# Kernel tuning notes

Hardware: AMD Instinct MI355X
Metric: run time of the kernel (lower is better)

The kernel has to match this reference:

```python
import jax, jax.numpy as jnp
import numpy as np

H, C, L = 2, 32, 25
EPS = 1e-5


def setup_inputs() -> dict:
    key = jax.random.key(0)
    ks = jax.random.split(key, 12)
    N, E = 20000, 100000
    x_input = jax.random.normal(ks[0], (N, 5), jnp.float32)
    # edges with no self loops (module uses add_self_loops=True, which first removes them)
    src = jax.random.randint(ks[1], (L, E), 0, N, dtype=jnp.int32)
    off = jax.random.randint(ks[2], (L, E), 1, N, dtype=jnp.int32)
    dst = (src + off) % N
    edge_indices = jnp.stack([src, dst], axis=1)              # [L, 2, E]
    edge_weights = jax.random.uniform(ks[3], (L, E, 1), jnp.float32)
    g = lambda k, shp, fan: jax.random.normal(k, shp, jnp.float32) / np.float32(np.sqrt(fan))
    return {
        "x_input": x_input,
        "edge_indices": edge_indices,
        "edge_weights": edge_weights,
        "Wl": g(ks[4], (L, 5, H * C), 5),
        "bl": jnp.zeros((L, H * C), jnp.float32),
        "Wr": g(ks[5], (L, 5, H * C), 5),
        "br": jnp.zeros((L, H * C), jnp.float32),
        "We": g(ks[6], (L, 1, H * C), 1),
        "att": g(ks[7], (L, H, C), C),
        "conv_bias": jnp.zeros((L, C), jnp.float32),
        "gamma1": jnp.ones((L, C), jnp.float32),
        "beta1": jnp.zeros((L, C), jnp.float32),
        "W1": g(ks[8], (800, 800), 800),
        "b1": jnp.zeros((800,), jnp.float32),
        "W2": g(ks[9], (800, 5), 800),
        "b2": jnp.zeros((5,), jnp.float32),
    }


def reference(x_input, edge_indices, edge_weights, Wl, bl, Wr, br, We, att,
              conv_bias, gamma1, beta1, W1, b1, W2, b2):
    N = x_input.shape[0]
    loops = jnp.arange(N, dtype=edge_indices.dtype)

    def layer(carry, p):
        ei, ew, wl, bl_, wr, br_, we, a, cb, g_, be_ = p
        src, dst = ei[0], ei[1]
        ones_e = jnp.ones((src.shape[0],), x_input.dtype)
        # add_self_loops with fill_value='mean': loop attr = mean of incoming edge attrs
        cnt = jax.ops.segment_sum(ones_e, dst, num_segments=N)
        loop_attr = jax.ops.segment_sum(ew, dst, num_segments=N) / jnp.maximum(cnt, 1.0)[:, None]
        s2 = jnp.concatenate([src, loops])
        d2 = jnp.concatenate([dst, loops])
        ea = jnp.concatenate([ew, loop_attr], axis=0)          # [E+N, 1]
        xl = (x_input @ wl + bl_).reshape(N, H, C)             # source transform
        xr = (x_input @ wr + br_).reshape(N, H, C)             # target transform
        eh = jax.nn.leaky_relu(xl[s2] + xr[d2] + (ea @ we).reshape(-1, H, C), 0.2)
        alpha = jnp.einsum('ehc,hc->eh', eh, a)                # [E+N, H]
        amax = jax.ops.segment_max(alpha, d2, num_segments=N)
        alpha = jnp.exp(alpha - amax[d2])
        alpha = alpha / jax.ops.segment_sum(alpha, d2, num_segments=N)[d2]
        msg = (xl[s2] * alpha[:, :, None]).reshape(-1, H * C)
        deg = jax.ops.segment_sum(jnp.ones((s2.shape[0],), x_input.dtype), d2, num_segments=N)
        out = (jax.ops.segment_sum(msg, d2, num_segments=N) / deg[:, None]).reshape(N, H, C)
        out = out.mean(axis=1) + cb                            # concat=False -> mean over heads, + bias
        mu = out.mean(axis=0)
        var = out.var(axis=0)                                  # BatchNorm1d, training-mode batch stats
        out = g_ * (out - mu) * jax.lax.rsqrt(var + EPS) + be_
        return carry, jax.nn.leaky_relu(out, 0.01)

    _, hs = jax.lax.scan(layer, None,
                         (edge_indices, edge_weights, Wl, bl, Wr, br, We, att,
                          conv_bias, gamma1, beta1))            # [L, N, C]
    h = jnp.transpose(hs, (1, 0, 2)).reshape(N, L * C)          # cat along feature dim
    h = jax.nn.relu(h @ W1 + b1)
    return h @ W2 + b2
```

## Files before the change

### kernel.cpp

```cpp
#include <hip/hip_runtime.h>
#include <hip/hip_bf16.h>

#define N_NODES 20000
#define N_EDGES 100000
#define N_LAYERS 25
#define NPAD 20096
#define EPS_BN 1e-5f
#define LOG2E 1.44269504088896340736f
#define NL_NN (N_LAYERS * N_NODES)
#define TOTAL_E (N_LAYERS * N_EDGES)
#define SCAN_BLKS ((NL_NN + 1023) / 1024)
#define QUARTER_N 5000
#define CNT_BLKS (N_LAYERS * 4)
#define W1T_END (CNT_BLKS + 700)
#define XPAD_END (W1T_END + 157)
#define HPAD_BLKS 75
#define PREP_BLKS (XPAD_END + HPAD_BLKS)
#define EDGE_BLKS ((TOTAL_E + 1023) / 1024)
#define FILL_BLKS (EDGE_BLKS + SCAN_BLKS)
#define NGRP 14
#define ATTN_BLKS (NL_NN / 4)
#define ATTN_PER_XCD (ATTN_BLKS / 8)

typedef short short8 __attribute__((ext_vector_type(8)));
typedef short short4v __attribute__((ext_vector_type(4)));
typedef float floatx4 __attribute__((ext_vector_type(4)));
typedef float float8v __attribute__((ext_vector_type(8)));
typedef int int8v __attribute__((ext_vector_type(8)));
typedef int int2v __attribute__((ext_vector_type(2)));

template <int PAT>
__device__ __forceinline__ float swz(float v) {
  return __int_as_float(__builtin_amdgcn_ds_swizzle(__float_as_int(v), PAT));
}

template <int CTRL>
__device__ __forceinline__ float dpp_add(float v) {
  int r = __builtin_amdgcn_update_dpp(0, __float_as_int(v), CTRL, 0xF, 0xF, true);
  return v + __int_as_float(r);
}

__device__ __forceinline__ float ldbf(const unsigned short* __restrict__ p, int idx) {
  return __uint_as_float((unsigned)p[idx] << 16);
}

__device__ __forceinline__ unsigned short bfbits(float v) {
  return __builtin_bit_cast(unsigned short, (__hip_bfloat16)v);
}

__device__ __forceinline__ void gl_lds16(const short* g, short* l) {
  __builtin_amdgcn_global_load_lds(
      (const __attribute__((address_space(1))) void*)g,
      (__attribute__((address_space(3))) void*)l, 16, 0, 0);
}

__device__ __forceinline__ int8v sload8(const void* p) {
  int8v r;
  asm volatile(
      "s_load_dwordx8 %0, %1, 0x0\n\t"
      "s_waitcnt lgkmcnt(0)"
      : "=s"(r)
      : "s"(p));
  return r;
}

__device__ __forceinline__ void sload2(const void* p, int& a, int& b) {
  int2v r;
  asm volatile(
      "s_load_dwordx2 %0, %1, 0x0\n\t"
      "s_waitcnt lgkmcnt(0)"
      : "=s"(r)
      : "s"(p));
  a = r[0];
  b = r[1];
}

__device__ __forceinline__ void sload_chunk(const void* p, int8v& r0, int8v& r1,
                                            int8v& r2, int8v& r3) {
  asm volatile(
      "s_load_dwordx8 %0, %4, 0x0\n\t"
      "s_load_dwordx8 %1, %4, 0x20\n\t"
      "s_load_dwordx8 %2, %4, 0x40\n\t"
      "s_load_dwordx8 %3, %4, 0x60\n\t"
      "s_waitcnt lgkmcnt(0)"
      : "=s"(r0), "=s"(r1), "=s"(r2), "=s"(r3)
      : "s"(p));
}

__device__ __forceinline__ void red4(float& p0, float& p1, float& p2, float& p3) {
  asm volatile(
      "s_nop 1\n\t"
      "v_add_f32_dpp %0, %0, %0 quad_perm:[1,0,3,2] row_mask:0xf bank_mask:0xf\n\t"
      "v_add_f32_dpp %1, %1, %1 quad_perm:[1,0,3,2] row_mask:0xf bank_mask:0xf\n\t"
      "v_add_f32_dpp %2, %2, %2 quad_perm:[1,0,3,2] row_mask:0xf bank_mask:0xf\n\t"
      "v_add_f32_dpp %3, %3, %3 quad_perm:[1,0,3,2] row_mask:0xf bank_mask:0xf\n\t"
      "v_add_f32_dpp %0, %0, %0 quad_perm:[2,3,0,1] row_mask:0xf bank_mask:0xf\n\t"
      "v_add_f32_dpp %1, %1, %1 quad_perm:[2,3,0,1] row_mask:0xf bank_mask:0xf\n\t"
      "v_add_f32_dpp %2, %2, %2 quad_perm:[2,3,0,1] row_mask:0xf bank_mask:0xf\n\t"
      "v_add_f32_dpp %3, %3, %3 quad_perm:[2,3,0,1] row_mask:0xf bank_mask:0xf\n\t"
      "v_add_f32_dpp %0, %0, %0 row_half_mirror row_mask:0xf bank_mask:0xf\n\t"
      "v_add_f32_dpp %1, %1, %1 row_half_mirror row_mask:0xf bank_mask:0xf\n\t"
      "v_add_f32_dpp %2, %2, %2 row_half_mirror row_mask:0xf bank_mask:0xf\n\t"
      "v_add_f32_dpp %3, %3, %3 row_half_mirror row_mask:0xf bank_mask:0xf\n\t"
      "v_add_f32_dpp %0, %0, %0 row_mirror row_mask:0xf bank_mask:0xf\n\t"
      "v_add_f32_dpp %1, %1, %1 row_mirror row_mask:0xf bank_mask:0xf\n\t"
      "v_add_f32_dpp %2, %2, %2 row_mirror row_mask:0xf bank_mask:0xf\n\t"
      "v_add_f32_dpp %3, %3, %3 row_mirror row_mask:0xf bank_mask:0xf\n\t"
      "s_nop 1"
      : "+v"(p0), "+v"(p1), "+v"(p2), "+v"(p3));
}

__device__ __forceinline__ float red1(float p) {
  asm volatile(
      "s_nop 1\n\t"
      "v_add_f32_dpp %0, %0, %0 quad_perm:[1,0,3,2] row_mask:0xf bank_mask:0xf\n\t"
      "s_nop 1\n\t"
      "v_add_f32_dpp %0, %0, %0 quad_perm:[2,3,0,1] row_mask:0xf bank_mask:0xf\n\t"
      "s_nop 1\n\t"
      "v_add_f32_dpp %0, %0, %0 row_half_mirror row_mask:0xf bank_mask:0xf\n\t"
      "s_nop 1\n\t"
      "v_add_f32_dpp %0, %0, %0 row_mirror row_mask:0xf bank_mask:0xf\n\t"
      "s_nop 1"
      : "+v"(p));
  return p;
}

__global__ __launch_bounds__(1024) void prep_kernel(
    const int* __restrict__ ei, const float* __restrict__ x,
    const float* __restrict__ W1, int* __restrict__ cnt,
    int* __restrict__ rank, float* __restrict__ xpad,
    __hip_bfloat16* __restrict__ W1bT, unsigned short* __restrict__ hn) {
  __shared__ int smem[QUARTER_N];
  int b = blockIdx.x;
  if (b < CNT_BLKS) {
    int l = b >> 2, base = (b & 3) * QUARTER_N;
    for (int i = threadIdx.x; i < QUARTER_N; i += 1024) smem[i] = 0;
    __syncthreads();
    const int* dstp = ei + (size_t)l * 2 * N_EDGES + N_EDGES;
    int* rkp = rank + l * N_EDGES;
    for (int e = threadIdx.x; e < N_EDGES; e += 1024) {
      int d = dstp[e] - base;
      if ((unsigned)d < (unsigned)QUARTER_N) rkp[e] = atomicAdd(&smem[d], 1);
    }
    __syncthreads();
    int* outp = cnt + l * N_NODES + base;
    for (int i = threadIdx.x; i < QUARTER_N; i += 1024) outp[i] = smem[i];
  } else if (b < W1T_END) {
    float* tile = (float*)smem;
    int bb = b - CNT_BLKS;
    int j0 = (bb % 28) * 32, k0 = (bb / 28) * 32;
    int tx = threadIdx.x & 31, ty = threadIdx.x >> 5;
    tile[ty * 33 + tx] = (j0 + tx < 800) ? W1[(k0 + ty) * 800 + j0 + tx] : 0.f;
    __syncthreads();
    W1bT[(size_t)(j0 + ty) * 800 + k0 + tx] = (__hip_bfloat16)tile[tx * 33 + ty];
  } else if (b < XPAD_END) {
    int idx = (b - W1T_END) * 1024 + threadIdx.x;
    if (idx < N_NODES * 8) {
      int nn = idx >> 3, k = idx & 7;
      xpad[idx] = (k < 5) ? x[nn * 5 + k] : 0.f;
    }
  } else {
    int idx = (b - XPAD_END) * 1024 + threadIdx.x;
    const int per_l = (NPAD - N_NODES) * 32;
    if (idx < N_LAYERS * per_l) {
      int l = idx / per_l;
      int rem = idx - l * per_l;
      hn[((size_t)l * NPAD + N_NODES) * 32 + rem] = 0;
    }
  }
}

__global__ __launch_bounds__(1024) void scan_a(const int* __restrict__ cnt,
                                               int* __restrict__ scn,
                                               int* __restrict__ btot,
                                               float* __restrict__ gsum,
                                               float* __restrict__ gsumsq) {
  int t = threadIdx.x, b = blockIdx.x;
  int i = b * 1024 + t;
  int lane = t & 63, wv = t >> 6;
  int v = (i < NL_NN) ? cnt[i] : 0;
  int sc = v;
#pragma unroll
  for (int off = 1; off < 64; off <<= 1) {
    int u = __shfl_up(sc, off);
    if (lane >= off) sc += u;
  }
  __shared__ int ws[16];
  if (lane == 63) ws[wv] = sc;
  __syncthreads();
  if (t < 16) {
    int xx = ws[t];
#pragma unroll
    for (int off = 1; off < 16; off <<= 1) {
      int u = __shfl_up(xx, off);
      if (t >= off) xx += u;
    }
    ws[t] = xx;
  }
  __syncthreads();
  int bofs = wv ? ws[wv - 1] : 0;
  if (i < NL_NN) scn[i] = bofs + sc - v;
  if (t == 0) btot[b] = ws[15];
  if (b == 200 && t < N_LAYERS * 32) {
    gsum[t] = 0.f;
    gsumsq[t] = 0.f;
  }
}

__global__ __launch_bounds__(512) void scan_b(const int* __restrict__ btot,
                                              int* __restrict__ boff) {
  int t = threadIdx.x;
  int lane = t & 63, wv = t >> 6;
  int v = (t < SCAN_BLKS) ? btot[t] : 0;
  int sc = v;
#pragma unroll
  for (int off = 1; off < 64; off <<= 1) {
    int u = __shfl_up(sc, off);
    if (lane >= off) sc += u;
  }
  __shared__ int ws[8];
  if (lane == 63) ws[wv] = sc;
  __syncthreads();
  if (t < 8) {
    int xx = ws[t];
#pragma unroll
    for (int off = 1; off < 8; off <<= 1) {
      int u = __shfl_up(xx, off);
      if (t >= off) xx += u;
    }
    ws[t] = xx;
  }
  __syncthreads();
  int bofs = wv ? ws[wv - 1] : 0;
  if (t < SCAN_BLKS) boff[t] = bofs + sc - v;
}

__global__ __launch_bounds__(1024) void fill_kernel(const int* __restrict__ ei,
                                                    const float* __restrict__ ew,
                                                    const int* __restrict__ scn,
                                                    const int* __restrict__ boff,
                                                    const int* __restrict__ rank,
                                                    const float* __restrict__ xpad,
                                                    int2* __restrict__ rowse,
                                                    float* __restrict__ epf) {
  int b = blockIdx.x;
  if (b < EDGE_BLKS) {
    int idx = b * 1024 + threadIdx.x;
    if (idx >= TOTAL_E) return;
    int l = idx / N_EDGES, e = idx - l * N_EDGES;
    int src = ei[(size_t)l * 2 * N_EDGES + e];
    int dst = ei[(size_t)l * 2 * N_EDGES + N_EDGES + e];
    int g = l * N_NODES + dst;
    int pos = scn[g] + boff[g >> 10] + rank[idx];
    float w = ew[(size_t)l * N_EDGES + e];
    float4 xv = *(const float4*)(xpad + (size_t)src * 8);
    float x4v = xpad[(size_t)src * 8 + 4];
    float8v r;
    r[0] = w; r[1] = xv.x; r[2] = xv.y; r[3] = xv.z; r[4] = xv.w; r[5] = x4v;
    r[6] = 0.f; r[7] = 0.f;
    *(float8v*)(epf + (size_t)pos * 8) = r;
  } else {
    int i = (b - EDGE_BLKS) * 1024 + threadIdx.x;
    if (i < NL_NN) {
      int st = scn[i] + boff[i >> 10];
      int en = (i + 1 < NL_NN) ? scn[i + 1] + boff[(i + 1) >> 10] : TOTAL_E;
      rowse[i] = make_int2(st, en);
    }
    if (i < 4) {
      float8v z = {0.f, 0.f, 0.f, 0.f, 0.f, 0.f, 0.f, 0.f};
      *(float8v*)(epf + (size_t)(TOTAL_E + i) * 8) = z;
    }
  }
}

__global__ __launch_bounds__(256) void attn_kernel(
    const float* __restrict__ xpad, const int2* __restrict__ rowse,
    const float* __restrict__ epf,
    const float* __restrict__ Wl, const float* __restrict__ bl,
    const float* __restrict__ Wr, const float* __restrict__ br,
    const float* __restrict__ We, const float* __restrict__ att,
    const float* __restrict__ cbias, unsigned short* __restrict__ out_pre) {
  int b = blockIdx.x;
  int nb = (b & 7) * ATTN_PER_XCD + (b >> 3);
  int wid = __builtin_amdgcn_readfirstlane(nb * 4 + (threadIdx.x >> 6));
  int lane = threadIdx.x & 63;
  int l = wid / N_NODES, n = wid - l * N_NODES;

  float wlv0 = Wl[(l * 5 + 0) * 64 + lane];
  float wlv1 = Wl[(l * 5 + 1) * 64 + lane];
  float wlv2 = Wl[(l * 5 + 2) * 64 + lane];
  float wlv3 = Wl[(l * 5 + 3) * 64 + lane];
  float wlv4 = Wl[(l * 5 + 4) * 64 + lane];
  float blv = bl[l * 64 + lane];
  float wev = We[l * 64 + lane];
  float att2v = att[l * 64 + lane] * LOG2E;

  int s_, e_;
  sload2(rowse + wid, s_, e_);
  int cnt = e_ - s_;

  int8v xn = sload8(xpad + (size_t)n * 8);
  float xrn = br[l * 64 + lane];
  float xln = blv;
  {
    float wr0 = Wr[(l * 5 + 0) * 64 + lane];
    float wr1 = Wr[(l * 5 + 1) * 64 + lane];
    float wr2 = Wr[(l * 5 + 2) * 64 + lane];
    float wr3 = Wr[(l * 5 + 3) * 64 + lane];
    float wr4 = Wr[(l * 5 + 4) * 64 + lane];
    float x0 = __int_as_float(xn[0]), x1 = __int_as_float(xn[1]);
    float x2 = __int_as_float(xn[2]), x3 = __int_as_float(xn[3]);
    float x4 = __int_as_float(xn[4]);
    xrn = fmaf(x0, wr0, xrn); xrn = fmaf(x1, wr1, xrn);
    xrn = fmaf(x2, wr2, xrn); xrn = fmaf(x3, wr3, xrn);
    xrn = fmaf(x4, wr4, xrn);
    xln = fmaf(x0, wlv0, xln); xln = fmaf(x1, wlv1, xln);
    xln = fmaf(x2, wlv2, xln); xln = fmaf(x3, wlv3, xln);
    xln = fmaf(x4, wlv4, xln);
  }

  float ssum = 0.f, acc = 0.f, ewsum = 0.f;
  int nchunk = (cnt + 3) >> 2;
  const float* pch = epf + (size_t)s_ * 8;
  for (int c = 0; c < nchunk; c++) {
    int8v r0, r1, r2, r3;
    sload_chunk(pch, r0, r1, r2, r3);
    pch += 32;
    int m = cnt - c * 4;
    float xa[4], pk[4], wv[4];
#pragma unroll
    for (int k = 0; k < 4; k++) {
      int8v rr = (k == 0) ? r0 : (k == 1) ? r1 : (k == 2) ? r2 : r3;
      bool ok = k < m;
      int wbits = ok ? rr[0] : 0;
      wv[k] = __int_as_float(wbits);
      float a = fmaf(__int_as_float(rr[1]), wlv0, blv);
      a = fmaf(__int_as_float(rr[2]), wlv1, a);
      a = fmaf(__int_as_float(rr[3]), wlv2, a);
      a = fmaf(__int_as_float(rr[4]), wlv3, a);
      a = fmaf(__int_as_float(rr[5]), wlv4, a);
      xa[k] = a;
      float bias = __int_as_float(ok ? 0 : (int)0xff800000);
      float v = a + fmaf(wv[k], wev, xrn);
      float lk = fmaxf(v, 0.2f * v);
      pk[k] = fmaf(lk, att2v, bias);
    }
    red4(pk[0], pk[1], pk[2], pk[3]);
#pragma unroll
    for (int k = 0; k < 4; k++) pk[k] += swz<0x401F>(pk[k]);
#pragma unroll
    for (int k = 0; k < 4; k++) {
      float pe = __builtin_amdgcn_exp2f(pk[k]);
      ssum += pe;
      acc = fmaf(xa[k], pe, acc);
      ewsum += wv[k];
    }
  }
  {
    float w = ewsum * __builtin_amdgcn_rcpf(fmaxf((float)cnt, 1.f));
    float v = xln + fmaf(w, wev, xrn);
    float lk = fmaxf(v, 0.2f * v);
    float p = red1(lk * att2v);
    p += swz<0x401F>(p);
    float pe = __builtin_amdgcn_exp2f(p);
    ssum += pe;
    acc = fmaf(xln, pe, acc);
  }
  float outv = acc * __builtin_amdgcn_rcpf(ssum * (float)(cnt + 1));
  float o2 = outv + __shfl_xor(outv, 32);
  if (lane < 32)
    out_pre[wid * 32 + lane] = bfbits(0.5f * o2 + cbias[l * 32 + lane]);
}

__global__ __launch_bounds__(256) void stats_kernel(const unsigned short* __restrict__ out_pre,
                                                    float* __restrict__ gsum,
                                                    float* __restrict__ gsumsq) {
  int l = blockIdx.x >> 4, chunk = blockIdx.x & 15;
  int t = threadIdx.x;
  int c = t & 31, nsub = t >> 5;
  int n0 = chunk * 1250;
  float s1 = 0.f, s2 = 0.f;
  for (int n = n0 + nsub; n < n0 + 1250; n += 8) {
    float v = ldbf(out_pre, (l * N_NODES + n) * 32 + c);
    s1 += v; s2 += v * v;
  }
  __shared__ float l1[256], l2[256];
  l1[t] = s1; l2[t] = s2;
  __syncthreads();
  for (int off = 128; off >= 32; off >>= 1) {
    if (t < off) { l1[t] += l1[t + off]; l2[t] += l2[t + off]; }
    __syncthreads();
  }
  if (t < 32) {
    atomicAdd(&gsum[l * 32 + t], l1[t]);
    atomicAdd(&gsumsq[l * 32 + t], l2[t]);
  }
}

__global__ __launch_bounds__(256) void norm_kernel(const unsigned short* __restrict__ out_pre,
                                                   const float* __restrict__ gsum,
                                                   const float* __restrict__ gsumsq,
                                                   const float* __restrict__ gamma,
                                                   const float* __restrict__ beta,
                                                   unsigned short* __restrict__ hn) {
  int idx = blockIdx.x * 256 + threadIdx.x;
  int l = idx / (N_NODES * 8);
  int rem = idx - l * (N_NODES * 8);
  int n = rem >> 3, q = rem & 7;
  int c0 = q * 4;
  short4v v4 = *(const short4v*)(out_pre + (l * N_NODES + n) * 32 + c0);
  short4v o;
#pragma unroll
  for (int i = 0; i < 4; i++) {
    int c = c0 + i;
    float mu = gsum[l * 32 + c] * (1.f / N_NODES);
    float var = gsumsq[l * 32 + c] * (1.f / N_NODES) - mu * mu;
    float vv = __uint_as_float((unsigned)(unsigned short)v4[i] << 16);
    float v = gamma[l * 32 + c] * (vv - mu) * rsqrtf(var + EPS_BN) + beta[l * 32 + c];
    v = v > 0.f ? v : 0.01f * v;
    o[i] = (short)bfbits(v);
  }
  *(short4v*)(hn + ((size_t)l * NPAD + n) * 32 + c0) = o;
}

__global__ __launch_bounds__(256) void gemm1_kernel(const short* __restrict__ hn,
                                                    const short* __restrict__ W1bT,
                                                    const float* __restrict__ b1,
                                                    const float* __restrict__ W2,
                                                    float* __restrict__ p) {
  __shared__ __align__(16) short As[128 * 32];
  __shared__ __align__(16) short Bs[128 * 32];
  int t = threadIdx.x;
  int n0 = blockIdx.x * 128, m0 = blockIdx.y * 128;
  int wave = t >> 6, lane = t & 63;
  int wr = wave >> 1, wc = wave & 1;
  int mrow = lane & 15, quad = lane >> 4;
  floatx4 acc[4][4];
#pragma unroll
  for (int i = 0; i < 4; i++)
#pragma unroll
    for (int j = 0; j < 4; j++) acc[i][j] = (floatx4){0.f, 0.f, 0.f, 0.f};

  int r0 = t >> 2, s0 = t & 3;
  int r1 = (t + 256) >> 2, s1 = (t + 256) & 3;
  const short* aG0 = hn + (m0 + r0) * 32 + s0 * 8;
  const short* aG1 = hn + (m0 + r1) * 32 + s1 * 8;
  const short* bG0 = W1bT + (n0 + r0) * 800 + s0 * 8;
  const short* bG1 = W1bT + (n0 + r1) * 800 + s1 * 8;
  const int ak = NPAD * 32;
  short* aD0 = As + wave * 512;
  short* aD1 = As + 2048 + wave * 512;
  short* bD0 = Bs + wave * 512;
  short* bD1 = Bs + 2048 + wave * 512;

  for (int kt = 0; kt < 25; kt++) {
    gl_lds16(aG0, aD0);
    gl_lds16(aG1, aD1);
    gl_lds16(bG0, bD0);
    gl_lds16(bG1, bD1);
    aG0 += ak; aG1 += ak; bG0 += 32; bG1 += 32;
    __syncthreads();
    short8 af[4], bfr[4];
#pragma unroll
    for (int i = 0; i < 4; i++)
      af[i] = *(const short8*)(&As[(wr * 64 + i * 16 + mrow) * 32 + quad * 8]);
#pragma unroll
    for (int j = 0; j < 4; j++)
      bfr[j] = *(const short8*)(&Bs[(wc * 64 + j * 16 + mrow) * 32 + quad * 8]);
#pragma unroll
    for (int i = 0; i < 4; i++)
#pragma unroll
      for (int j = 0; j < 4; j++)
        acc[i][j] = __builtin_amdgcn_mfma_f32_16x16x32_bf16(af[i], bfr[j], acc[i][j], 0, 0, 0);
    __syncthreads();
  }

  float w2v[4][5];
  float b1v[4];
#pragma unroll
  for (int j = 0; j < 4; j++) {
    int col = n0 + wc * 64 + j * 16 + mrow;
    bool ok = col < 800;
    b1v[j] = ok ? b1[col] : 0.f;
#pragma unroll
    for (int jj = 0; jj < 5; jj++) w2v[j][jj] = ok ? W2[col * 5 + jj] : 0.f;
  }
  int grp = blockIdx.x * 2 + wc;
#pragma unroll
  for (int i = 0; i < 4; i++) {
#pragma unroll
    for (int r = 0; r < 4; r++) {
      float s[5] = {0.f, 0.f, 0.f, 0.f, 0.f};
#pragma unroll
      for (int j = 0; j < 4; j++) {
        float v = fmaxf(acc[i][j][r] + b1v[j], 0.f);
#pragma unroll
        for (int jj = 0; jj < 5; jj++) s[jj] = fmaf(v, w2v[j][jj], s[jj]);
      }
#pragma unroll
      for (int jj = 0; jj < 5; jj++) {
        s[jj] = dpp_add<0xB1>(s[jj]);
        s[jj] = dpp_add<0x4E>(s[jj]);
        s[jj] = dpp_add<0x141>(s[jj]);
        s[jj] = dpp_add<0x140>(s[jj]);
      }
      int row = m0 + wr * 64 + i * 16 + quad * 4 + r;
      if (mrow == 0) {
#pragma unroll
        for (int jj = 0; jj < 5; jj++)
          p[(row * NGRP + grp) * 5 + jj] = s[jj];
      }
    }
  }
}

__global__ __launch_bounds__(256) void gemm2r_kernel(const float* __restrict__ p,
                                                     const float* __restrict__ b2,
                                                     float* __restrict__ out) {
  int idx = blockIdx.x * 256 + threadIdx.x;
  if (idx >= N_NODES * 5) return;
  int row = idx / 5, jj = idx - row * 5;
  float s = b2[jj];
#pragma unroll
  for (int g = 0; g < NGRP; g++) s += p[(row * NGRP + g) * 5 + jj];
  out[idx] = s;
}

extern "C" void kernel_launch(void* const* d_in, const int* in_sizes, int n_in,
                              void* d_out, int out_size, void* d_ws, size_t ws_size,
                              hipStream_t stream) {
  const float* x    = (const float*)d_in[0];
  const int*   ei   = (const int*)d_in[1];
  const float* ew   = (const float*)d_in[2];
  const float* Wl   = (const float*)d_in[3];
  const float* bl   = (const float*)d_in[4];
  const float* Wr   = (const float*)d_in[5];
  const float* br   = (const float*)d_in[6];
  const float* We   = (const float*)d_in[7];
  const float* att  = (const float*)d_in[8];
  const float* cb   = (const float*)d_in[9];
  const float* gam  = (const float*)d_in[10];
  const float* bet  = (const float*)d_in[11];
  const float* W1   = (const float*)d_in[12];
  const float* b1   = (const float*)d_in[13];
  const float* W2   = (const float*)d_in[14];
  const float* b2   = (const float*)d_in[15];

  char* ws = (char*)d_ws;
  size_t off = 0;
  auto alloc = [&](size_t bytes) {
    void* p = ws + off;
    off = (off + bytes + 255) & ~(size_t)255;
    return p;
  };
  int* cnt     = (int*)alloc((size_t)NL_NN * 4);
  int* scn     = (int*)alloc((size_t)NL_NN * 4);
  int* btot    = (int*)alloc(SCAN_BLKS * 4);
  int* boff    = (int*)alloc(SCAN_BLKS * 4);
  int* rank    = (int*)alloc((size_t)TOTAL_E * 4);
  int2* rowse  = (int2*)alloc((size_t)NL_NN * 8);
  float* epf   = (float*)alloc((size_t)TOTAL_E * 32 + 128);
  unsigned short* out_pre = (unsigned short*)alloc((size_t)NL_NN * 32 * 2);
  float* gsum   = (float*)alloc(N_LAYERS * 32 * 4);
  float* gsumsq = (float*)alloc(N_LAYERS * 32 * 4);
  float* xpad   = (float*)alloc((size_t)N_NODES * 8 * 4);
  __hip_bfloat16* w1t = (__hip_bfloat16*)alloc((size_t)896 * 800 * 2);
  float* pbuf = (float*)alloc((size_t)NPAD * NGRP * 5 * 4);
  unsigned short* hn = (unsigned short*)alloc((size_t)N_LAYERS * NPAD * 32 * 2);

  prep_kernel<<<PREP_BLKS, 1024, 0, stream>>>(ei, x, W1, cnt, rank, xpad, w1t, hn);
  scan_a<<<SCAN_BLKS, 1024, 0, stream>>>(cnt, scn, btot, gsum, gsumsq);
  scan_b<<<1, 512, 0, stream>>>(btot, boff);
  fill_kernel<<<FILL_BLKS, 1024, 0, stream>>>(ei, ew, scn, boff, rank, xpad,
                                              rowse, epf);
  attn_kernel<<<ATTN_BLKS, 256, 0, stream>>>(
      xpad, rowse, epf, Wl, bl, Wr, br, We, att, cb, out_pre);
  stats_kernel<<<N_LAYERS * 16, 256, 0, stream>>>(out_pre, gsum, gsumsq);
  norm_kernel<<<(NL_NN * 8) / 256, 256, 0, stream>>>(
      out_pre, gsum, gsumsq, gam, bet, hn);
  gemm1_kernel<<<dim3(7, 157), 256, 0, stream>>>(
      (const short*)hn, (const short*)w1t, b1, W2, pbuf);
  gemm2r_kernel<<<(N_NODES * 5 + 255) / 256, 256, 0, stream>>>(
      pbuf, b2, (float*)d_out);
}
```

Before: 500.5 us.

## Process eight destination nodes per wave in attention kernel with CSR rowptr

```diff
diff --git a/kernel.cpp b/kernel.cpp
--- a/kernel.cpp
+++ b/kernel.cpp
@@ -19,8 +19,10 @@
 #define EDGE_BLKS ((TOTAL_E + 1023) / 1024)
 #define FILL_BLKS (EDGE_BLKS + SCAN_BLKS)
 #define NGRP 14
-#define ATTN_BLKS (NL_NN / 4)
-#define ATTN_PER_XCD (ATTN_BLKS / 8)
+#define NPW 8
+#define NPL (N_NODES / NPW)
+#define ATTN_WAVES (NL_NN / NPW)
+#define ATTN_BLKS (ATTN_WAVES / 4)
 
 typedef short short8 __attribute__((ext_vector_type(8)));
 typedef short short4v __attribute__((ext_vector_type(4)));
@@ -64,15 +66,13 @@
   return r;
 }
 
-__device__ __forceinline__ void sload2(const void* p, int& a, int& b) {
-  int2v r;
+__device__ __forceinline__ void sload_rp(const void* p, int8v& a, int8v& b) {
   asm volatile(
-      "s_load_dwordx2 %0, %1, 0x0\n\t"
+      "s_load_dwordx8 %0, %2, 0x0\n\t"
+      "s_load_dwordx8 %1, %2, 0x20\n\t"
       "s_waitcnt lgkmcnt(0)"
-      : "=s"(r)
+      : "=s"(a), "=s"(b)
       : "s"(p));
-  a = r[0];
-  b = r[1];
 }
 
 __device__ __forceinline__ void sload_chunk(const void* p, int8v& r0, int8v& r1,
@@ -241,7 +241,7 @@
                                                     const int* __restrict__ boff,
                                                     const int* __restrict__ rank,
                                                     const float* __restrict__ xpad,
-                                                    int2* __restrict__ rowse,
+                                                    int* __restrict__ rowptr,
                                                     float* __restrict__ epf) {
   int b = blockIdx.x;
   if (b < EDGE_BLKS) {
@@ -261,11 +261,8 @@
     *(float8v*)(epf + (size_t)pos * 8) = r;
   } else {
     int i = (b - EDGE_BLKS) * 1024 + threadIdx.x;
-    if (i < NL_NN) {
-      int st = scn[i] + boff[i >> 10];
-      int en = (i + 1 < NL_NN) ? scn[i + 1] + boff[(i + 1) >> 10] : TOTAL_E;
-      rowse[i] = make_int2(st, en);
-    }
+    if (i < NL_NN) rowptr[i] = scn[i] + boff[i >> 10];
+    if (i < 31) rowptr[NL_NN + i] = TOTAL_E;
     if (i < 4) {
       float8v z = {0.f, 0.f, 0.f, 0.f, 0.f, 0.f, 0.f, 0.f};
       *(float8v*)(epf + (size_t)(TOTAL_E + i) * 8) = z;
@@ -274,102 +271,110 @@
 }
 
 __global__ __launch_bounds__(256) void attn_kernel(
-    const float* __restrict__ xpad, const int2* __restrict__ rowse,
+    const float* __restrict__ xpad, const int* __restrict__ rowptr,
     const float* __restrict__ epf,
     const float* __restrict__ Wl, const float* __restrict__ bl,
     const float* __restrict__ Wr, const float* __restrict__ br,
     const float* __restrict__ We, const float* __restrict__ att,
     const float* __restrict__ cbias, unsigned short* __restrict__ out_pre) {
   int b = blockIdx.x;
-  int nb = (b & 7) * ATTN_PER_XCD + (b >> 3);
+  const int q = ATTN_BLKS >> 3, r = ATTN_BLKS & 7;
+  int xcd = b & 7, ib = b >> 3;
+  int nb = (xcd < r ? xcd * (q + 1) : r * (q + 1) + (xcd - r) * q) + ib;
   int wid = __builtin_amdgcn_readfirstlane(nb * 4 + (threadIdx.x >> 6));
   int lane = threadIdx.x & 63;
-  int l = wid / N_NODES, n = wid - l * N_NODES;
+  int l = wid / NPL;
+  int n0 = (wid - l * NPL) * NPW;
 
   float wlv0 = Wl[(l * 5 + 0) * 64 + lane];
   float wlv1 = Wl[(l * 5 + 1) * 64 + lane];
   float wlv2 = Wl[(l * 5 + 2) * 64 + lane];
   float wlv3 = Wl[(l * 5 + 3) * 64 + lane];
   float wlv4 = Wl[(l * 5 + 4) * 64 + lane];
+  float wr0 = Wr[(l * 5 + 0) * 64 + lane];
+  float wr1 = Wr[(l * 5 + 1) * 64 + lane];
+  float wr2 = Wr[(l * 5 + 2) * 64 + lane];
+  float wr3 = Wr[(l * 5 + 3) * 64 + lane];
+  float wr4 = Wr[(l * 5 + 4) * 64 + lane];
   float blv = bl[l * 64 + lane];
+  float brv = br[l * 64 + lane];
   float wev = We[l * 64 + lane];
   float att2v = att[l * 64 + lane] * LOG2E;
-
-  int s_, e_;
-  sload2(rowse + wid, s_, e_);
-  int cnt = e_ - s_;
-
-  int8v xn = sload8(xpad + (size_t)n * 8);
-  float xrn = br[l * 64 + lane];
-  float xln = blv;
-  {
-    float wr0 = Wr[(l * 5 + 0) * 64 + lane];
-    float wr1 = Wr[(l * 5 + 1) * 64 + lane];
-    float wr2 = Wr[(l * 5 + 2) * 64 + lane];
-    float wr3 = Wr[(l * 5 + 3) * 64 + lane];
-    float wr4 = Wr[(l * 5 + 4) * 64 + lane];
+  float cbv = cbias[l * 32 + (lane & 31)];
+
+  int8v rpa, rpb;
+  sload_rp(rowptr + (size_t)wid * 8, rpa, rpb);
+
+#pragma unroll
+  for (int i = 0; i < NPW; i++) {
+    int st = rpa[i & 7];
+    int en = (i == 7) ? rpb[0] : rpa[(i + 1) & 7];
+    int cnt = en - st;
+
+    int8v xn = sload8(xpad + (size_t)(n0 + i) * 8);
     float x0 = __int_as_float(xn[0]), x1 = __int_as_float(xn[1]);
     float x2 = __int_as_float(xn[2]), x3 = __int_as_float(xn[3]);
     float x4 = __int_as_float(xn[4]);
+    float xrn = brv, xln = blv;
     xrn = fmaf(x0, wr0, xrn); xrn = fmaf(x1, wr1, xrn);
     xrn = fmaf(x2, wr2, xrn); xrn = fmaf(x3, wr3, xrn);
     xrn = fmaf(x4, wr4, xrn);
     xln = fmaf(x0, wlv0, xln); xln = fmaf(x1, wlv1, xln);
     xln = fmaf(x2, wlv2, xln); xln = fmaf(x3, wlv3, xln);
     xln = fmaf(x4, wlv4, xln);
-  }
-
-  float ssum = 0.f, acc = 0.f, ewsum = 0.f;
-  int nchunk = (cnt + 3) >> 2;
-  const float* pch = epf + (size_t)s_ * 8;
-  for (int c = 0; c < nchunk; c++) {
-    int8v r0, r1, r2, r3;
-    sload_chunk(pch, r0, r1, r2, r3);
-    pch += 32;
-    int m = cnt - c * 4;
-    float xa[4], pk[4], wv[4];
-#pragma unroll
-    for (int k = 0; k < 4; k++) {
-      int8v rr = (k == 0) ? r0 : (k == 1) ? r1 : (k == 2) ? r2 : r3;
-      bool ok = k < m;
-      int wbits = ok ? rr[0] : 0;
-      wv[k] = __int_as_float(wbits);
-      float a = fmaf(__int_as_float(rr[1]), wlv0, blv);
-      a = fmaf(__int_as_float(rr[2]), wlv1, a);
-      a = fmaf(__int_as_float(rr[3]), wlv2, a);
-      a = fmaf(__int_as_float(rr[4]), wlv3, a);
-      a = fmaf(__int_as_float(rr[5]), wlv4, a);
-      xa[k] = a;
-      float bias = __int_as_float(ok ? 0 : (int)0xff800000);
-      float v = a + fmaf(wv[k], wev, xrn);
+
+    float ssum = 0.f, acc = 0.f, ewsum = 0.f;
+    int nchunk = (cnt + 3) >> 2;
+    const float* pch = epf + (size_t)st * 8;
+    for (int c = 0; c < nchunk; c++) {
+      int8v r0, r1, r2, r3;
+      sload_chunk(pch, r0, r1, r2, r3);
+      pch += 32;
+      int m = cnt - c * 4;
+      float xa[4], pk[4], wv[4];
+#pragma unroll
+      for (int k = 0; k < 4; k++) {
+        int8v rr = (k == 0) ? r0 : (k == 1) ? r1 : (k == 2) ? r2 : r3;
+        bool ok = k < m;
+        int wbits = ok ? rr[0] : 0;
+        wv[k] = __int_as_float(wbits);
+        float a = fmaf(__int_as_float(rr[1]), wlv0, blv);
+        a = fmaf(__int_as_float(rr[2]), wlv1, a);
+        a = fmaf(__int_as_float(rr[3]), wlv2, a);
+        a = fmaf(__int_as_float(rr[4]), wlv3, a);
+        a = fmaf(__int_as_float(rr[5]), wlv4, a);
+        xa[k] = a;
+        float bias = __int_as_float(ok ? 0 : (int)0xff800000);
+        float v = a + fmaf(wv[k], wev, xrn);
+        float lk = fmaxf(v, 0.2f * v);
+        pk[k] = fmaf(lk, att2v, bias);
+      }
+      red4(pk[0], pk[1], pk[2], pk[3]);
+#pragma unroll
+      for (int k = 0; k < 4; k++) pk[k] += swz<0x401F>(pk[k]);
+#pragma unroll
+      for (int k = 0; k < 4; k++) {
+        float pe = __builtin_amdgcn_exp2f(pk[k]);
+        ssum += pe;
+        acc = fmaf(xa[k], pe, acc);
+        ewsum += wv[k];
+      }
+    }
+    {
+      float w = ewsum * __builtin_amdgcn_rcpf(fmaxf((float)cnt, 1.f));
+      float v = xln + fmaf(w, wev, xrn);
       float lk = fmaxf(v, 0.2f * v);
-      pk[k] = fmaf(lk, att2v, bias);
-    }
-    red4(pk[0], pk[1], pk[2], pk[3]);
-#pragma unroll
-    for (int k = 0; k < 4; k++) pk[k] += swz<0x401F>(pk[k]);
-#pragma unroll
-    for (int k = 0; k < 4; k++) {
-      float pe = __builtin_amdgcn_exp2f(pk[k]);
+      float p = red1(lk * att2v);
+      p += swz<0x401F>(p);
+      float pe = __builtin_amdgcn_exp2f(p);
       ssum += pe;
-      acc = fmaf(xa[k], pe, acc);
-      ewsum += wv[k];
-    }
-  }
-  {
-    float w = ewsum * __builtin_amdgcn_rcpf(fmaxf((float)cnt, 1.f));
-    float v = xln + fmaf(w, wev, xrn);
-    float lk = fmaxf(v, 0.2f * v);
-    float p = red1(lk * att2v);
-    p += swz<0x401F>(p);
-    float pe = __builtin_amdgcn_exp2f(p);
-    ssum += pe;
-    acc = fmaf(xln, pe, acc);
-  }
-  float outv = acc * __builtin_amdgcn_rcpf(ssum * (float)(cnt + 1));
-  float o2 = outv + __shfl_xor(outv, 32);
-  if (lane < 32)
-    out_pre[wid * 32 + lane] = bfbits(0.5f * o2 + cbias[l * 32 + lane]);
+      acc = fmaf(xln, pe, acc);
+    }
+    float outv = acc * __builtin_amdgcn_rcpf(ssum * (float)(cnt + 1));
+    float o2 = outv + __shfl_xor(outv, 32);
+    if (lane < 32)
+      out_pre[((size_t)wid * NPW + i) * 32 + lane] = bfbits(0.5f * o2 + cbv);
+  }
 }
 
 __global__ __launch_bounds__(256) void stats_kernel(const unsigned short* __restrict__ out_pre,
@@ -558,7 +563,7 @@
   int* btot    = (int*)alloc(SCAN_BLKS * 4);
   int* boff    = (int*)alloc(SCAN_BLKS * 4);
   int* rank    = (int*)alloc((size_t)TOTAL_E * 4);
-  int2* rowse  = (int2*)alloc((size_t)NL_NN * 8);
+  int* rowptr  = (int*)alloc((size_t)(NL_NN + 32) * 4);
   float* epf   = (float*)alloc((size_t)TOTAL_E * 32 + 128);
   unsigned short* out_pre = (unsigned short*)alloc((size_t)NL_NN * 32 * 2);
   float* gsum   = (float*)alloc(N_LAYERS * 32 * 4);
@@ -572,9 +577,9 @@
   scan_a<<<SCAN_BLKS, 1024, 0, stream>>>(cnt, scn, btot, gsum, gsumsq);
   scan_b<<<1, 512, 0, stream>>>(btot, boff);
   fill_kernel<<<FILL_BLKS, 1024, 0, stream>>>(ei, ew, scn, boff, rank, xpad,
-                                              rowse, epf);
+                                              rowptr, epf);
   attn_kernel<<<ATTN_BLKS, 256, 0, stream>>>(
-      xpad, rowse, epf, Wl, bl, Wr, br, We, att, cb, out_pre);
+      xpad, rowptr, epf, Wl, bl, Wr, br, We, att, cb, out_pre);
   stats_kernel<<<N_LAYERS * 16, 256, 0, stream>>>(out_pre, gsum, gsumsq);
   norm_kernel<<<(NL_NN * 8) / 256, 256, 0, stream>>>(
       out_pre, gsum, gsumsq, gam, bet, hn);
```

New measurement: 496.7 us. About the same (-0.8%).
